# Kernel tuning notes

Hardware: AMD Instinct MI355X
Metric: run time of the kernel (lower is better)

## Reference

```python
import jax, jax.numpy as jnp
import numpy as np
import math

BLOCK = 256
NUM_HEADS = 32
HEAD_DIM = 128
HIDDEN = 2048
INNER = NUM_HEADS * HEAD_DIM
SEQ = 4096
EPS = 1e-5
LAYER_IDX = 0
NUM_LAYERS = 32


def _build_slopes(n):
    def get_slopes(n):
        def pow2(m):
            start = 2 ** (-2 ** (-(math.log2(m) - 3)))
            return [start * start ** i for i in range(m)]
        if math.log2(n).is_integer():
            return pow2(n)
        c = 2 ** math.floor(math.log2(n))
        return pow2(c) + get_slopes(2 * c)[0::2][: n - c]
    s = np.asarray(get_slopes(n), dtype=np.float32).reshape(n, 1, 1)
    # layer decay scaling as in __init__
    s = s * (1.0 - LAYER_IDX / (NUM_LAYERS - 1) + 1e-5)
    return s


def setup_inputs() -> dict:
    key = jax.random.key(0)
    k1, k2, k3, k4 = jax.random.split(key, 4)
    sd_h = 1.0 / math.sqrt(HIDDEN)
    sd_i = 1.0 / math.sqrt(INNER)
    return {
        "hidden_states": jax.random.normal(k1, (SEQ, HIDDEN), jnp.float32),
        "w_qkv": jax.random.normal(k2, (HIDDEN, 3 * INNER), jnp.float32) * sd_h,
        "w_gate": jax.random.normal(k3, (HIDDEN, INNER), jnp.float32) * sd_h,
        "w_out": jax.random.normal(k4, (INNER, HIDDEN), jnp.float32) * sd_i,
        "norm_weight": jnp.ones((INNER,), jnp.float32),
        "slope_rate": jnp.asarray(_build_slopes(NUM_HEADS)),
        "kv_cache": jnp.zeros((NUM_HEADS, HEAD_DIM, HEAD_DIM), jnp.float32),
    }


def _lightning_attention(q, k, v, slope, kv0):
    # q,k,v: [h, n, d]; slope: [h,1,1]; kv0: [h, d, d]
    h, n, d = q.shape
    nb = n // BLOCK
    qb = q.reshape(h, nb, BLOCK, d).transpose(1, 0, 2, 3)  # [nb,h,B,d]
    kb = k.reshape(h, nb, BLOCK, d).transpose(1, 0, 2, 3)
    vb = v.reshape(h, nb, BLOCK, d).transpose(1, 0, 2, 3)

    idx = jnp.arange(BLOCK, dtype=jnp.float32)
    diff = idx[:, None] - idx[None, :]                      # i - j
    s = slope.reshape(h, 1, 1)
    intra_decay = jnp.where(diff >= 0, jnp.exp(-s * diff), 0.0)   # [h,B,B]
    q_decay = jnp.exp(-s * (idx + 1.0).reshape(1, BLOCK, 1))      # [h,B,1]
    k_decay = jnp.exp(-s * (BLOCK - 1.0 - idx).reshape(1, BLOCK, 1))  # [h,B,1]
    block_decay = jnp.exp(-s * BLOCK)                             # [h,1,1]

    def step(kv, blk):
        qc, kc, vc = blk  # each [h,B,d]
        scores = jnp.einsum('hid,hjd->hij', qc, kc) * intra_decay
        o_intra = jnp.einsum('hij,hjd->hid', scores, vc)
        o_inter = q_decay * jnp.einsum('hid,hde->hie', qc, kv)
        kv_new = block_decay * kv + jnp.einsum('hjd,hje->hde', kc * k_decay, vc)
        return kv_new, o_intra + o_inter

    kv_final, outs = jax.lax.scan(step, kv0, (qb, kb, vb))
    out = outs.transpose(1, 0, 2, 3).reshape(h, n, d)
    return out, kv_final


def reference(hidden_states, w_qkv, w_gate, w_out, norm_weight, slope_rate, kv_cache):
    n = hidden_states.shape[0]
    # qkv projection + SiLU activation (done in fp32 in the original)
    qkv = jax.nn.silu(hidden_states @ w_qkv)                  # [n, 3*inner]
    qkv = qkv.reshape(n, NUM_HEADS, 3 * HEAD_DIM)
    q, k, v = jnp.split(qkv, 3, axis=-1)                      # [n,h,d] each
    q = q.transpose(1, 0, 2)                                  # [h,n,d]
    k = k.transpose(1, 0, 2)
    v = v.transpose(1, 0, 2)

    attn, kv_final = _lightning_attention(q, k, v, slope_rate, kv_cache)
    attn = attn.transpose(1, 0, 2).reshape(n, INNER)          # n (h d)

    # RMSNorm (fp32) then sigmoid gate then output projection
    var = jnp.mean(attn * attn, axis=-1, keepdims=True)
    normed = attn * jax.lax.rsqrt(var + EPS) * norm_weight
    gate = jax.nn.sigmoid(hidden_states @ w_gate)
    out = (gate * normed) @ w_out                             # [n, hidden]
    return out
```

## Files before the change

kernel.cpp:

```cpp
#include <hip/hip_runtime.h>
#include <stdint.h>

typedef __bf16 bf16x8 __attribute__((ext_vector_type(8)));
typedef float  f32x4  __attribute__((ext_vector_type(4)));
typedef unsigned short u16x8 __attribute__((ext_vector_type(8)));

__device__ __forceinline__ unsigned short f2bf(float f) {
    union { float f; uint32_t u; } x; x.f = f;
    uint32_t r = (x.u + 0x7FFFu + ((x.u >> 16) & 1u)) >> 16;
    return (unsigned short)r;
}
__device__ __forceinline__ float bf2f(unsigned short b) {
    union { uint32_t u; float f; } x; x.u = ((uint32_t)b) << 16;
    return x.f;
}

__device__ __forceinline__ void gl16(const void* g, void* l) {
    __builtin_amdgcn_global_load_lds(
        (const __attribute__((address_space(1))) void*)g,
        (__attribute__((address_space(3))) void*)(uint32_t)(uintptr_t)l,
        16, 0, 0);
}

#define MFMA16(a, b, c) __builtin_amdgcn_mfma_f32_16x16x32_bf16((a), (b), (c), 0, 0, 0)

__global__ __launch_bounds__(256) void f32_to_bf16_kernel(const float* __restrict__ in,
                                                          unsigned short* __restrict__ out,
                                                          int n8) {
    int i = blockIdx.x * 256 + threadIdx.x;
    if (i >= n8) return;
    float4 a = ((const float4*)in)[2 * i];
    float4 b = ((const float4*)in)[2 * i + 1];
    u16x8 o;
    o[0] = f2bf(a.x); o[1] = f2bf(a.y); o[2] = f2bf(a.z); o[3] = f2bf(a.w);
    o[4] = f2bf(b.x); o[5] = f2bf(b.y); o[6] = f2bf(b.z); o[7] = f2bf(b.w);
    ((u16x8*)out)[i] = o;
}

__global__ __launch_bounds__(256) void transpose_w_kernel(const float* __restrict__ in,
                                                          unsigned short* __restrict__ out,
                                                          int R, int C) {
    __shared__ float tile[64][65];
    int c0 = blockIdx.x * 64, r0 = blockIdx.y * 64;
    int tid = threadIdx.x;
    int tr = tid >> 4;
    int tc4 = (tid & 15) * 4;
#pragma unroll
    for (int it = 0; it < 4; ++it) {
        int r = it * 16 + tr;
        float4 v = *(const float4*)&in[(size_t)(r0 + r) * C + c0 + tc4];
        tile[r][tc4] = v.x; tile[r][tc4 + 1] = v.y;
        tile[r][tc4 + 2] = v.z; tile[r][tc4 + 3] = v.w;
    }
    __syncthreads();
#pragma unroll
    for (int it = 0; it < 4; ++it) {
        int c = it * 16 + tr;
        ushort4 o;
        o.x = f2bf(tile[tc4][c]);
        o.y = f2bf(tile[tc4 + 1][c]);
        o.z = f2bf(tile[tc4 + 2][c]);
        o.w = f2bf(tile[tc4 + 3][c]);
        *(ushort4*)&out[(size_t)(c0 + c) * R + r0 + tc4] = o;
    }
}

__global__ __launch_bounds__(512, 2) void gemm_qkvgate_kernel(const unsigned short* __restrict__ A,
                                                              const unsigned short* __restrict__ Bt,
                                                              unsigned short* __restrict__ qkvp,
                                                              unsigned short* __restrict__ gatep,
                                                              int K, int NBN, int NQ) {
    __shared__ unsigned short Abuf[2][2][8192];
    __shared__ unsigned short Bbuf[2][2][8192];

    int bid = blockIdx.x;
    int xcd = bid & 7, kw = bid >> 3;
    int bm = (xcd & 3) * 4 + (kw & 3);
    int bn = (xcd >> 2) * (NBN >> 1) + (kw >> 2);
    int tid = threadIdx.x, lane = tid & 63, w = tid >> 6;
    int wr = w >> 2, wc = w & 3;

    int r0 = tid >> 3;
    int cbs = (tid & 7) << 4;
    int el0 = (cbs ^ ((r0 & 7) << 4)) >> 1;
    int r1 = 64 + r0;
    int el1 = (cbs ^ ((r1 & 7) << 4)) >> 1;
    int lo0 = tid * 16, lo1 = 8192 + tid * 16;

    const unsigned short* Ag0 = A + (size_t)(bm * 256) * K;
    const unsigned short* Ag1 = A + (size_t)(bm * 256 + 128) * K;
    const unsigned short* Bg0 = Bt + (size_t)(bn * 256) * K;
    const unsigned short* Bg1 = Bt + (size_t)(bn * 256 + 128) * K;

#define STAGE(src, dstHalf, k0)                                            \
    do {                                                                   \
        gl16((src) + (size_t)r0 * K + (k0) + el0, (char*)(dstHalf) + lo0); \
        gl16((src) + (size_t)r1 * K + (k0) + el1, (char*)(dstHalf) + lo1); \
    } while (0)

    int aRow = wr * 64 + (lane & 15);
    int bRow = wc * 32 + (lane & 15);
    int swz = (lane & 7) << 4;
    int cbb = (lane >> 4) << 4;

#define RD_A(slot, R, m, kk) \
    af[R][m][kk] = *(const bf16x8*)((const char*)Abuf[slot][R] + ((aRow + (m) * 16) << 7) + (((kk) * 64 + cbb) ^ swz))
#define RD_B(slot, Cq, n, kk) \
    bfr[Cq][n][kk] = *(const bf16x8*)((const char*)Bbuf[slot][Cq] + ((bRow + (n) * 16) << 7) + (((kk) * 64 + cbb) ^ swz))

#define QUAD(q, Rh, Cc)                                                       \
    do {                                                                      \
        _Pragma("unroll")                                                     \
        for (int m = 0; m < 4; ++m)                                           \
            _Pragma("unroll")                                                 \
            for (int n = 0; n < 2; ++n) {                                     \
                acc[q][m][n] = MFMA16(af[Rh][m][0], bfr[Cc][n][0], acc[q][m][n]); \
                acc[q][m][n] = MFMA16(af[Rh][m][1], bfr[Cc][n][1], acc[q][m][n]); \
            }                                                                 \
    } while (0)

    bf16x8 af[2][4][2];
    bf16x8 bfr[2][2][2];
    f32x4 acc[4][4][2];
#pragma unroll
    for (int q = 0; q < 4; ++q)
#pragma unroll
        for (int m = 0; m < 4; ++m)
#pragma unroll
            for (int n = 0; n < 2; ++n)
#pragma unroll
                for (int r = 0; r < 4; ++r) acc[q][m][n][r] = 0.f;

    int NT = K >> 6;
    STAGE(Ag0, Abuf[0][0], 0);
    STAGE(Bg0, Bbuf[0][0], 0);
    STAGE(Ag1, Abuf[0][1], 0);
    STAGE(Bg1, Bbuf[0][1], 0);
    STAGE(Ag0, Abuf[1][0], 64);
    STAGE(Bg0, Bbuf[1][0], 64);
    STAGE(Ag1, Abuf[1][1], 64);
    STAGE(Bg1, Bbuf[1][1], 64);
    asm volatile("s_waitcnt vmcnt(8)" ::: "memory");
    __builtin_amdgcn_s_barrier();
#pragma unroll
    for (int m = 0; m < 4; ++m) { RD_A(0, 0, m, 0); RD_A(0, 0, m, 1); }
#pragma unroll
    for (int n = 0; n < 2; ++n) { RD_B(0, 0, n, 0); RD_B(0, 0, n, 1); }

    for (int t = 0; t < NT; ++t) {
        int cur = t & 1, nx = cur ^ 1;
        bool rd = (t + 1 < NT);
        bool st = (t + 2 < NT);
        int ks = (t + 2) << 6;

#pragma unroll
        for (int m = 0; m < 4; ++m) { RD_A(cur, 1, m, 0); RD_A(cur, 1, m, 1); }
        asm volatile("s_waitcnt lgkmcnt(8)" ::: "memory");
        __builtin_amdgcn_sched_barrier(0);
        __builtin_amdgcn_s_setprio(1);
        QUAD(0, 0, 0);
        __builtin_amdgcn_s_setprio(0);

#pragma unroll
        for (int n = 0; n < 2; ++n) { RD_B(cur, 1, n, 0); RD_B(cur, 1, n, 1); }
        asm volatile("s_waitcnt lgkmcnt(4)" ::: "memory");
        __builtin_amdgcn_sched_barrier(0);
        __builtin_amdgcn_s_setprio(1);
        QUAD(1, 1, 0);
        __builtin_amdgcn_s_setprio(0);

        asm volatile("s_waitcnt lgkmcnt(0)" ::: "memory");
        asm volatile("s_waitcnt vmcnt(0)" ::: "memory");
        __builtin_amdgcn_s_barrier();
        if (st) {
            STAGE(Ag0, Abuf[cur][0], ks);
            STAGE(Bg0, Bbuf[cur][0], ks);
        }
        if (rd) {
#pragma unroll
            for (int n = 0; n < 2; ++n) { RD_B(nx, 0, n, 0); RD_B(nx, 0, n, 1); }
        }
        __builtin_amdgcn_s_setprio(1);
        QUAD(2, 0, 1);
        __builtin_amdgcn_s_setprio(0);

        if (st) {
            STAGE(Ag1, Abuf[cur][1], ks);
            STAGE(Bg1, Bbuf[cur][1], ks);
        }
        if (rd) {
#pragma unroll
            for (int m = 0; m < 4; ++m) { RD_A(nx, 0, m, 0); RD_A(nx, 0, m, 1); }
        }
        __builtin_amdgcn_s_setprio(1);
        QUAD(3, 1, 1);
        __builtin_amdgcn_s_setprio(0);
    }

    bool isQ = (bn < NQ);
    unsigned short* outp = isQ ? qkvp : gatep;
    int Nout = isQ ? 12288 : 4096;
    int colb0 = (isQ ? bn : bn - NQ) * 256;
#pragma unroll
    for (int q = 0; q < 4; ++q) {
        const int R_ = q & 1, C_ = q >> 1;
#pragma unroll
        for (int m = 0; m < 4; ++m) {
            int row0 = bm * 256 + R_ * 128 + wr * 64 + m * 16 + ((lane >> 4) * 4);
#pragma unroll
            for (int n = 0; n < 2; ++n) {
                int col = colb0 + C_ * 128 + wc * 32 + n * 16 + (lane & 15);
#pragma unroll
                for (int rg = 0; rg < 4; ++rg) {
                    float v = acc[q][m][n][rg];
                    float sig = 1.f / (1.f + __expf(-v));
                    float r = isQ ? v * sig : sig;
                    outp[(size_t)(row0 + rg) * Nout + col] = f2bf(r);
                }
            }
        }
    }
#undef STAGE
#undef RD_A
#undef RD_B
#undef QUAD
}

template <int ACT, int OUTBF>
__global__ __launch_bounds__(256) void gemm_bt_kernel(const unsigned short* __restrict__ A,
                                                      const unsigned short* __restrict__ Bt,
                                                      void* __restrict__ Cp,
                                                      int M, int N, int K) {
    __shared__ unsigned short As[128 * 64];
    __shared__ unsigned short Bs[128 * 64];
    int bn = blockIdx.x, bm = blockIdx.y;
    int tid = threadIdx.x, lane = tid & 63, w = tid >> 6;
    int wr = w >> 1, wc = w & 1;

    f32x4 acc[4][4];
#pragma unroll
    for (int m = 0; m < 4; ++m)
#pragma unroll
        for (int n = 0; n < 4; ++n)
#pragma unroll
            for (int r = 0; r < 4; ++r) acc[m][n][r] = 0.f;

    const size_t Abase = (size_t)bm * 128 * K;
    const size_t Bbase = (size_t)bn * 128 * K;

    for (int k0 = 0; k0 < K; k0 += 64) {
        __syncthreads();
#pragma unroll
        for (int it = 0; it < 4; ++it) {
            int slot = it * 256 + tid;
            int o = slot * 16;
            int r = o >> 7;
            int cb = o & 127;
            int scb = cb ^ ((r & 7) << 4);
            gl16(A + Abase + (size_t)r * K + k0 + (scb >> 1), (char*)As + o);
            gl16(Bt + Bbase + (size_t)r * K + k0 + (scb >> 1), (char*)Bs + o);
        }
        __syncthreads();
#pragma unroll
        for (int kk = 0; kk < 2; ++kk) {
            int kb = kk * 64 + ((lane >> 4) * 16);
            bf16x8 af[4], bfr[4];
#pragma unroll
            for (int m = 0; m < 4; ++m) {
                int r = wr * 64 + m * 16 + (lane & 15);
                af[m] = *(const bf16x8*)((const char*)As + (r << 7) + (kb ^ ((r & 7) << 4)));
            }
#pragma unroll
            for (int n = 0; n < 4; ++n) {
                int r = wc * 64 + n * 16 + (lane & 15);
                bfr[n] = *(const bf16x8*)((const char*)Bs + (r << 7) + (kb ^ ((r & 7) << 4)));
            }
#pragma unroll
            for (int m = 0; m < 4; ++m)
#pragma unroll
                for (int n = 0; n < 4; ++n)
                    acc[m][n] = MFMA16(af[m], bfr[n], acc[m][n]);
        }
    }

#pragma unroll
    for (int m = 0; m < 4; ++m) {
        int rowb = bm * 128 + wr * 64 + m * 16 + ((lane >> 4) * 4);
#pragma unroll
        for (int n = 0; n < 4; ++n) {
            int col = bn * 128 + wc * 64 + n * 16 + (lane & 15);
#pragma unroll
            for (int r = 0; r < 4; ++r) {
                float v = acc[m][n][r];
                if (ACT == 1) v = v / (1.f + __expf(-v));
                else if (ACT == 2) v = 1.f / (1.f + __expf(-v));
                size_t idx = (size_t)(rowb + r) * N + col;
                if (OUTBF) ((unsigned short*)Cp)[idx] = f2bf(v);
                else       ((float*)Cp)[idx] = v;
            }
        }
    }
}

__global__ __launch_bounds__(256) void kv_transpose_kernel(const unsigned short* __restrict__ qkv,
                                                           const float* __restrict__ slopes,
                                                           unsigned short* __restrict__ kts,
                                                           unsigned short* __restrict__ vt) {
    __shared__ unsigned short tk[32][33];
    __shared__ unsigned short tv[32][33];
    int n0 = blockIdx.x * 32, d0 = blockIdx.y * 32, h = blockIdx.z;
    float s = slopes[h];
    int lx = threadIdx.x & 31, ly = threadIdx.x >> 5;
#pragma unroll
    for (int i = ly; i < 32; i += 8) {
        int n = n0 + i;
        size_t rowb = (size_t)n * 12288 + h * 384;
        float kv = bf2f(qkv[rowb + 128 + d0 + lx]) * __expf(-s * (float)(255 - (n & 255)));
        tk[i][lx] = f2bf(kv);
        tv[i][lx] = qkv[rowb + 256 + d0 + lx];
    }
    __syncthreads();
#pragma unroll
    for (int i = ly; i < 32; i += 8) {
        size_t ob = (size_t)(h * 128 + d0 + i) * 4096 + n0 + lx;
        kts[ob] = tk[lx][i];
        vt[ob] = tv[lx][i];
    }
}

__global__ __launch_bounds__(256) void kv_outer_kernel(const unsigned short* __restrict__ kts,
                                                       const unsigned short* __restrict__ vt,
                                                       float* __restrict__ U) {
    __shared__ unsigned short Kc[128 * 64];
    __shared__ unsigned short Vc[128 * 64];
    int blk = blockIdx.x;
    int h = blk & 31, t = blk >> 5;
    int tid = threadIdx.x, lane = tid & 63, w = tid >> 6;

    f32x4 acc[2][8];
#pragma unroll
    for (int m = 0; m < 2; ++m)
#pragma unroll
        for (int n = 0; n < 8; ++n)
#pragma unroll
            for (int r = 0; r < 4; ++r) acc[m][n][r] = 0.f;

    for (int ks = 0; ks < 4; ++ks) {
        __syncthreads();
#pragma unroll
        for (int it = 0; it < 4; ++it) {
            int slot = it * 256 + tid;
            int o = slot * 16;
            int r = o >> 7;
            int cb = o & 127;
            int scb = cb ^ ((r & 7) << 4);
            size_t j = (size_t)t * 256 + ks * 64 + (scb >> 1);
            gl16(kts + (size_t)(h * 128 + r) * 4096 + j, (char*)Kc + o);
            gl16(vt + (size_t)(h * 128 + r) * 4096 + j, (char*)Vc + o);
        }
        __syncthreads();
#pragma unroll
        for (int kk = 0; kk < 2; ++kk) {
            int kb = kk * 64 + ((lane >> 4) * 16);
            bf16x8 vf[2], kf[8];
#pragma unroll
            for (int m = 0; m < 2; ++m) {
                int e = w * 32 + m * 16 + (lane & 15);
                vf[m] = *(const bf16x8*)((const char*)Vc + (e << 7) + (kb ^ ((e & 7) << 4)));
            }
#pragma unroll
            for (int n = 0; n < 8; ++n) {
                int d = n * 16 + (lane & 15);
                kf[n] = *(const bf16x8*)((const char*)Kc + (d << 7) + (kb ^ ((d & 7) << 4)));
            }
#pragma unroll
            for (int m = 0; m < 2; ++m)
#pragma unroll
                for (int n = 0; n < 8; ++n)
                    acc[m][n] = MFMA16(vf[m], kf[n], acc[m][n]);
        }
    }
    size_t base = (size_t)(h * 16 + t) * 16384;
#pragma unroll
    for (int m = 0; m < 2; ++m)
#pragma unroll
        for (int n = 0; n < 8; ++n)
#pragma unroll
            for (int r = 0; r < 4; ++r) {
                int e = w * 32 + m * 16 + ((lane >> 4) * 4) + r;
                int d = n * 16 + (lane & 15);
                U[base + (size_t)e * 128 + d] = acc[m][n][r];
            }
}

__global__ __launch_bounds__(256) void kv_scan_kernel(const float* __restrict__ kv_cache,
                                                      const float* __restrict__ U,
                                                      const float* __restrict__ slopes,
                                                      unsigned short* __restrict__ Wb) {
    __shared__ float Tt[16][132];
    int h = blockIdx.x >> 3;
    int c = blockIdx.x & 7;
    int c0 = c * 2048, e0 = c * 16;
    int tid = threadIdx.x;
    float s = slopes[h];
    float bd = __expf(-s * 256.f);
    size_t hb = (size_t)h * 16384;
#pragma unroll
    for (int it = 0; it < 8; ++it) {
        int d = it * 16 + (tid >> 4);
        Tt[tid & 15][d] = kv_cache[hb + (size_t)d * 128 + e0 + (tid & 15)];
    }
    __syncthreads();
    float wst[8];
#pragma unroll
    for (int i = 0; i < 8; ++i) {
        int e_rel = i * 2 + (tid >> 7);
        wst[i] = Tt[e_rel][tid & 127];
    }
    for (int t = 0; t < 16; ++t) {
        size_t base = (size_t)(h * 16 + t) * 16384 + c0;
#pragma unroll
        for (int i = 0; i < 8; ++i) {
            int idx = i * 256 + tid;
            Wb[base + idx] = f2bf(wst[i]);
            wst[i] = bd * wst[i] + U[base + idx];
        }
    }
}

__global__ __launch_bounds__(256, 2) void attn_out_kernel(const unsigned short* __restrict__ qkv,
                                                          const unsigned short* __restrict__ vt,
                                                          const unsigned short* __restrict__ Wb,
                                                          const float* __restrict__ slopes,
                                                          unsigned short* __restrict__ attn) {
    __shared__ unsigned short lds[40960];
    unsigned short* Qs = lds;
    unsigned short* Ps = lds + 16384;
    unsigned short* KW = lds + 24576;
    unsigned short* Ks = KW;
    unsigned short* Vs = KW + 8192;

    int blk = blockIdx.x;
    int h = blk & 31, tq = blk >> 5;
    int t = tq >> 1, qh = tq & 1;
    float s = slopes[h];
    int tid = threadIdx.x, lane = tid & 63, w = tid >> 6;
    int rowbase = t * 256 + qh * 128;

#pragma unroll
    for (int it = 0; it < 8; ++it) {
        int o = (it * 256 + tid) * 16;
        int r = o >> 8, cb = o & 255, scb = cb ^ ((r & 7) << 4);
        gl16(qkv + (size_t)(rowbase + r) * 12288 + h * 384 + (scb >> 1), (char*)Qs + o);
    }
#pragma unroll
    for (int it = 0; it < 8; ++it) {
        int o = (it * 256 + tid) * 16;
        int e = o >> 8, cb = o & 255, scb = cb ^ ((e & 7) << 4);
        gl16(Wb + (size_t)((h * 16 + t) * 128 + e) * 128 + (scb >> 1), (char*)KW + o);
    }
    __syncthreads();

    f32x4 acc[2][8];
#pragma unroll
    for (int m = 0; m < 2; ++m)
#pragma unroll
        for (int n = 0; n < 8; ++n)
#pragma unroll
            for (int r = 0; r < 4; ++r) acc[m][n][r] = 0.f;

#pragma unroll
    for (int kk = 0; kk < 4; ++kk) {
        int kb = kk * 64 + ((lane >> 4) * 16);
        bf16x8 qf[2], wf[8];
#pragma unroll
        for (int m = 0; m < 2; ++m) {
            int r = w * 32 + m * 16 + (lane & 15);
            qf[m] = *(const bf16x8*)((const char*)Qs + (r << 8) + (kb ^ ((r & 7) << 4)));
        }
#pragma unroll
        for (int n = 0; n < 8; ++n) {
            int e = n * 16 + (lane & 15);
            wf[n] = *(const bf16x8*)((const char*)KW + (e << 8) + (kb ^ ((e & 7) << 4)));
        }
#pragma unroll
        for (int m = 0; m < 2; ++m)
#pragma unroll
            for (int n = 0; n < 8; ++n)
                acc[m][n] = MFMA16(qf[m], wf[n], acc[m][n]);
    }
#pragma unroll
    for (int m = 0; m < 2; ++m)
#pragma unroll
        for (int rg = 0; rg < 4; ++rg) {
            int i = qh * 128 + w * 32 + m * 16 + ((lane >> 4) * 4) + rg;
            float qd = __expf(-s * (float)(i + 1));
#pragma unroll
            for (int n = 0; n < 8; ++n) acc[m][n][rg] *= qd;
        }

    int jbmax = ((qh << 2) + w) >> 1;
    for (int jb = 0; jb < 4; ++jb) {
        __syncthreads();
#pragma unroll
        for (int it = 0; it < 4; ++it) {
            int o = (it * 256 + tid) * 16;
            int r = o >> 8, cb = o & 255, scb = cb ^ ((r & 7) << 4);
            gl16(qkv + (size_t)(t * 256 + jb * 64 + r) * 12288 + h * 384 + 128 + (scb >> 1),
                 (char*)Ks + o);
        }
#pragma unroll
        for (int it = 0; it < 4; ++it) {
            int o = (it * 256 + tid) * 16;
            int e = o >> 7, cb = o & 127, scb = cb ^ ((e & 7) << 4);
            gl16(vt + (size_t)(h * 128 + e) * 4096 + t * 256 + jb * 64 + (scb >> 1),
                 (char*)Vs + o);
        }
        __syncthreads();

        if (jb <= jbmax) {
            f32x4 sc[2][4];
#pragma unroll
            for (int m = 0; m < 2; ++m)
#pragma unroll
                for (int n = 0; n < 4; ++n)
#pragma unroll
                    for (int r = 0; r < 4; ++r) sc[m][n][r] = 0.f;
#pragma unroll
            for (int kk = 0; kk < 4; ++kk) {
                int kb = kk * 64 + ((lane >> 4) * 16);
                bf16x8 qf[2], kf[4];
#pragma unroll
                for (int m = 0; m < 2; ++m) {
                    int r = w * 32 + m * 16 + (lane & 15);
                    qf[m] = *(const bf16x8*)((const char*)Qs + (r << 8) + (kb ^ ((r & 7) << 4)));
                }
#pragma unroll
                for (int n = 0; n < 4; ++n) {
                    int r = n * 16 + (lane & 15);
                    kf[n] = *(const bf16x8*)((const char*)Ks + (r << 8) + (kb ^ ((r & 7) << 4)));
                }
#pragma unroll
                for (int m = 0; m < 2; ++m)
#pragma unroll
                    for (int n = 0; n < 4; ++n)
                        sc[m][n] = MFMA16(qf[m], kf[n], sc[m][n]);
            }
            unsigned short* Pw = Ps + w * 2048;
#pragma unroll
            for (int m = 0; m < 2; ++m)
#pragma unroll
                for (int n = 0; n < 4; ++n)
#pragma unroll
                    for (int rg = 0; rg < 4; ++rg) {
                        int il = m * 16 + ((lane >> 4) * 4) + rg;
                        int i = qh * 128 + w * 32 + il;
                        int jl = n * 16 + (lane & 15);
                        int j = jb * 64 + jl;
                        float v = 0.f;
                        if (i >= j) v = sc[m][n][rg] * __expf(-s * (float)(i - j));
                        int cb2 = (jl * 2) ^ ((il & 7) << 4);
                        *(unsigned short*)((char*)Pw + (il << 7) + cb2) = f2bf(v);
                    }
            asm volatile("s_waitcnt lgkmcnt(0)" ::: "memory");
#pragma unroll
            for (int kk = 0; kk < 2; ++kk) {
                int kb = kk * 64 + ((lane >> 4) * 16);
                bf16x8 pf[2], vf[8];
#pragma unroll
                for (int m = 0; m < 2; ++m) {
                    int il = m * 16 + (lane & 15);
                    pf[m] = *(const bf16x8*)((const char*)Pw + (il << 7) + (kb ^ ((il & 7) << 4)));
                }
#pragma unroll
                for (int n = 0; n < 8; ++n) {
                    int e = n * 16 + (lane & 15);
                    vf[n] = *(const bf16x8*)((const char*)Vs + (e << 7) + (kb ^ ((e & 7) << 4)));
                }
#pragma unroll
                for (int m = 0; m < 2; ++m)
#pragma unroll
                    for (int n = 0; n < 8; ++n)
                        acc[m][n] = MFMA16(pf[m], vf[n], acc[m][n]);
            }
        }
    }

#pragma unroll
    for (int m = 0; m < 2; ++m)
#pragma unroll
        for (int n = 0; n < 8; ++n)
#pragma unroll
            for (int rg = 0; rg < 4; ++rg) {
                int i = qh * 128 + w * 32 + m * 16 + ((lane >> 4) * 4) + rg;
                int col = h * 128 + n * 16 + (lane & 15);
                attn[(size_t)(t * 256 + i) * 4096 + col] = f2bf(acc[m][n][rg]);
            }
}

__global__ __launch_bounds__(256) void rms_gate_kernel(const unsigned short* __restrict__ attn,
                                                       const unsigned short* __restrict__ gate,
                                                       const float* __restrict__ nw,
                                                       unsigned short* __restrict__ gated) {
    int row = blockIdx.x, tid = threadIdx.x;
    int lane = tid & 63, w = tid >> 6;
    const unsigned short* ar = attn + (size_t)row * 4096 + tid * 16;
    u16x8 a0 = *(const u16x8*)ar;
    u16x8 a1 = *(const u16x8*)(ar + 8);
    float v[16];
    float ss = 0.f;
#pragma unroll
    for (int j = 0; j < 8; ++j) { v[j] = bf2f(a0[j]); v[8 + j] = bf2f(a1[j]); }
#pragma unroll
    for (int j = 0; j < 16; ++j) ss += v[j] * v[j];
#pragma unroll
    for (int o = 32; o > 0; o >>= 1) ss += __shfl_xor(ss, o);
    __shared__ float red[4];
    if (lane == 0) red[w] = ss;
    __syncthreads();
    float tot = red[0] + red[1] + red[2] + red[3];
    float rs = rsqrtf(tot * (1.f / 4096.f) + 1e-5f);
    const unsigned short* gr = gate + (size_t)row * 4096 + tid * 16;
    u16x8 g0 = *(const u16x8*)gr;
    u16x8 g1 = *(const u16x8*)(gr + 8);
    const float* nwp = nw + tid * 16;
    u16x8 o0, o1;
#pragma unroll
    for (int j = 0; j < 8; ++j) {
        o0[j] = f2bf(v[j] * rs * nwp[j] * bf2f(g0[j]));
        o1[j] = f2bf(v[8 + j] * rs * nwp[8 + j] * bf2f(g1[j]));
    }
    unsigned short* gp = gated + (size_t)row * 4096 + tid * 16;
    *(u16x8*)gp = o0;
    *(u16x8*)(gp + 8) = o1;
}

extern "C" void kernel_launch(void* const* d_in, const int* in_sizes, int n_in,
                              void* d_out, int out_size, void* d_ws, size_t ws_size,
                              hipStream_t stream) {
    const float* hs       = (const float*)d_in[0];
    const float* w_qkv    = (const float*)d_in[1];
    const float* w_gate   = (const float*)d_in[2];
    const float* w_out    = (const float*)d_in[3];
    const float* nw       = (const float*)d_in[4];
    const float* slopes   = (const float*)d_in[5];
    const float* kv_cache = (const float*)d_in[6];
    float* out = (float*)d_out;
    char* ws = (char*)d_ws;

    unsigned short* hsb  = (unsigned short*)(ws + 0);
    unsigned short* wqt  = (unsigned short*)(ws + 16777216);
    unsigned short* wgt  = (unsigned short*)(ws + 67108864);
    unsigned short* wot  = (unsigned short*)(ws + 83886080);
    unsigned short* qkv  = (unsigned short*)(ws + 100663296);
    unsigned short* gate = (unsigned short*)(ws + 201326592);
    unsigned short* kts  = (unsigned short*)(ws + 234881024);
    unsigned short* vt   = (unsigned short*)(ws + 268435456);
    float*          U    = (float*)(ws + 301989888);
    unsigned short* Wb   = (unsigned short*)(ws + 335544320);
    unsigned short* attn  = wqt;
    unsigned short* gated = qkv;

    f32_to_bf16_kernel<<<4096, 256, 0, stream>>>(hs, hsb, 1048576);
    {
        dim3 g(192, 32);
        transpose_w_kernel<<<g, 256, 0, stream>>>(w_qkv, wqt, 2048, 12288);
    }
    {
        dim3 g(64, 32);
        transpose_w_kernel<<<g, 256, 0, stream>>>(w_gate, wgt, 2048, 4096);
    }
    {
        dim3 g(32, 64);
        transpose_w_kernel<<<g, 256, 0, stream>>>(w_out, wot, 4096, 2048);
    }
    gemm_qkvgate_kernel<<<1024, 512, 0, stream>>>(hsb, wqt, qkv, gate, 2048, 64, 48);
    {
        dim3 g(128, 4, 32);
        kv_transpose_kernel<<<g, 256, 0, stream>>>(qkv, slopes, kts, vt);
    }
    kv_outer_kernel<<<512, 256, 0, stream>>>(kts, vt, U);
    kv_scan_kernel<<<256, 256, 0, stream>>>(kv_cache, U, slopes, Wb);
    attn_out_kernel<<<1024, 256, 0, stream>>>(qkv, vt, Wb, slopes, attn);
    rms_gate_kernel<<<4096, 256, 0, stream>>>(attn, gate, nw, gated);
    {
        dim3 g(16, 32);
        gemm_bt_kernel<0, 0><<<g, 256, 0, stream>>>(gated, wot, out, 4096, 2048, 4096);
    }
}
```

Baseline: 507.5 us.

## Pipeline output GEMM with double-buffered LDS and relax waitcnts in QKV GEMM

Replaces the simple single-buffered output projection GEMM with a double-buffered, quadrant-split kernel. It prefetches the next K tiles via global_load_lds while MFMAs run, raises occupancy to two blocks per CU, and remaps workgroup ids with an XCD-aware swizzle. In the fused QKV/gate GEMM, the full vmcnt(0) drain is replaced by partial waits plus an extra barrier at loop top, so loads for the next stage stay in flight longer. The added synchronisation and tighter vmcnt counting risk race conditions if the counts are off.

```diff
diff --git a/kernel.cpp b/kernel.cpp
--- a/kernel.cpp
+++ b/kernel.cpp
@@ -153,6 +153,12 @@
         bool st = (t + 2 < NT);
         int ks = (t + 2) << 6;
 
+        if (t) {
+            if (rd) asm volatile("s_waitcnt vmcnt(8)" ::: "memory");
+            else    asm volatile("s_waitcnt vmcnt(0)" ::: "memory");
+            __builtin_amdgcn_s_barrier();
+            __builtin_amdgcn_sched_barrier(0);
+        }
 #pragma unroll
         for (int m = 0; m < 4; ++m) { RD_A(cur, 1, m, 0); RD_A(cur, 1, m, 1); }
         asm volatile("s_waitcnt lgkmcnt(8)" ::: "memory");
@@ -170,8 +176,10 @@
         __builtin_amdgcn_s_setprio(0);
 
         asm volatile("s_waitcnt lgkmcnt(0)" ::: "memory");
-        asm volatile("s_waitcnt vmcnt(0)" ::: "memory");
+        if (rd) asm volatile("s_waitcnt vmcnt(4)" ::: "memory");
+        else    asm volatile("s_waitcnt vmcnt(0)" ::: "memory");
         __builtin_amdgcn_s_barrier();
+        __builtin_amdgcn_sched_barrier(0);
         if (st) {
             STAGE(Ag0, Abuf[cur][0], ks);
             STAGE(Bg0, Bbuf[cur][0], ks);
@@ -226,80 +234,163 @@
 #undef QUAD
 }
 
-template <int ACT, int OUTBF>
-__global__ __launch_bounds__(256) void gemm_bt_kernel(const unsigned short* __restrict__ A,
-                                                      const unsigned short* __restrict__ Bt,
-                                                      void* __restrict__ Cp,
-                                                      int M, int N, int K) {
-    __shared__ unsigned short As[128 * 64];
-    __shared__ unsigned short Bs[128 * 64];
-    int bn = blockIdx.x, bm = blockIdx.y;
+__global__ __launch_bounds__(256, 2) void gemm_out_kernel(const unsigned short* __restrict__ A,
+                                                          const unsigned short* __restrict__ Bt,
+                                                          float* __restrict__ Cout,
+                                                          int N, int K, int NBN) {
+    __shared__ unsigned short Abuf[2][2][4096];
+    __shared__ unsigned short Bbuf[2][2][4096];
+
+    int bid = blockIdx.x, nwg = gridDim.x;
+    int wg = (bid & 7) * (nwg >> 3) + (bid >> 3);
+    int bm = wg / NBN, bn = wg % NBN;
     int tid = threadIdx.x, lane = tid & 63, w = tid >> 6;
     int wr = w >> 1, wc = w & 1;
 
-    f32x4 acc[4][4];
-#pragma unroll
-    for (int m = 0; m < 4; ++m)
-#pragma unroll
-        for (int n = 0; n < 4; ++n)
-#pragma unroll
-            for (int r = 0; r < 4; ++r) acc[m][n][r] = 0.f;
-
-    const size_t Abase = (size_t)bm * 128 * K;
-    const size_t Bbase = (size_t)bn * 128 * K;
-
-    for (int k0 = 0; k0 < K; k0 += 64) {
-        __syncthreads();
-#pragma unroll
-        for (int it = 0; it < 4; ++it) {
-            int slot = it * 256 + tid;
-            int o = slot * 16;
-            int r = o >> 7;
-            int cb = o & 127;
-            int scb = cb ^ ((r & 7) << 4);
-            gl16(A + Abase + (size_t)r * K + k0 + (scb >> 1), (char*)As + o);
-            gl16(Bt + Bbase + (size_t)r * K + k0 + (scb >> 1), (char*)Bs + o);
-        }
-        __syncthreads();
-#pragma unroll
-        for (int kk = 0; kk < 2; ++kk) {
-            int kb = kk * 64 + ((lane >> 4) * 16);
-            bf16x8 af[4], bfr[4];
-#pragma unroll
-            for (int m = 0; m < 4; ++m) {
-                int r = wr * 64 + m * 16 + (lane & 15);
-                af[m] = *(const bf16x8*)((const char*)As + (r << 7) + (kb ^ ((r & 7) << 4)));
+    int r0 = tid >> 3;
+    int cbs = (tid & 7) << 4;
+    int el0 = (cbs ^ ((r0 & 7) << 4)) >> 1;
+    int r1 = 32 + r0;
+    int el1 = (cbs ^ ((r1 & 7) << 4)) >> 1;
+    int lo0 = tid * 16, lo1 = 4096 + tid * 16;
+
+    const unsigned short* Ag0 = A + (size_t)(bm * 128) * K;
+    const unsigned short* Ag1 = A + (size_t)(bm * 128 + 64) * K;
+    const unsigned short* Bg0 = Bt + (size_t)(bn * 128) * K;
+    const unsigned short* Bg1 = Bt + (size_t)(bn * 128 + 64) * K;
+
+#define STAGE(src, dstHalf, k0)                                            \
+    do {                                                                   \
+        gl16((src) + (size_t)r0 * K + (k0) + el0, (char*)(dstHalf) + lo0); \
+        gl16((src) + (size_t)r1 * K + (k0) + el1, (char*)(dstHalf) + lo1); \
+    } while (0)
+
+    int aRow = wr * 32 + (lane & 15);
+    int bRow = wc * 32 + (lane & 15);
+    int swz = (lane & 7) << 4;
+    int cbb = (lane >> 4) << 4;
+
+#define RD_A(slot, R, m, kk) \
+    af[R][m][kk] = *(const bf16x8*)((const char*)Abuf[slot][R] + ((aRow + (m) * 16) << 7) + (((kk) * 64 + cbb) ^ swz))
+#define RD_B(slot, Cq, n, kk) \
+    bfr[Cq][n][kk] = *(const bf16x8*)((const char*)Bbuf[slot][Cq] + ((bRow + (n) * 16) << 7) + (((kk) * 64 + cbb) ^ swz))
+
+#define QUAD(q, Rh, Cc)                                                       \
+    do {                                                                      \
+        _Pragma("unroll")                                                     \
+        for (int m = 0; m < 2; ++m)                                           \
+            _Pragma("unroll")                                                 \
+            for (int n = 0; n < 2; ++n) {                                     \
+                acc[q][m][n] = MFMA16(af[Rh][m][0], bfr[Cc][n][0], acc[q][m][n]); \
+                acc[q][m][n] = MFMA16(af[Rh][m][1], bfr[Cc][n][1], acc[q][m][n]); \
+            }                                                                 \
+    } while (0)
+
+    bf16x8 af[2][2][2];
+    bf16x8 bfr[2][2][2];
+    f32x4 acc[4][2][2];
+#pragma unroll
+    for (int q = 0; q < 4; ++q)
+#pragma unroll
+        for (int m = 0; m < 2; ++m)
+#pragma unroll
+            for (int n = 0; n < 2; ++n)
+#pragma unroll
+                for (int r = 0; r < 4; ++r) acc[q][m][n][r] = 0.f;
+
+    int NT = K >> 6;
+    STAGE(Ag0, Abuf[0][0], 0);
+    STAGE(Bg0, Bbuf[0][0], 0);
+    STAGE(Ag1, Abuf[0][1], 0);
+    STAGE(Bg1, Bbuf[0][1], 0);
+    STAGE(Ag0, Abuf[1][0], 64);
+    STAGE(Bg0, Bbuf[1][0], 64);
+    STAGE(Ag1, Abuf[1][1], 64);
+    STAGE(Bg1, Bbuf[1][1], 64);
+    asm volatile("s_waitcnt vmcnt(8)" ::: "memory");
+    __builtin_amdgcn_s_barrier();
+#pragma unroll
+    for (int m = 0; m < 2; ++m) { RD_A(0, 0, m, 0); RD_A(0, 0, m, 1); }
+#pragma unroll
+    for (int n = 0; n < 2; ++n) { RD_B(0, 0, n, 0); RD_B(0, 0, n, 1); }
+
+    for (int t = 0; t < NT; ++t) {
+        int cur = t & 1, nx = cur ^ 1;
+        bool rd = (t + 1 < NT);
+        bool st = (t + 2 < NT);
+        int ks = (t + 2) << 6;
+
+        if (t) {
+            if (rd) asm volatile("s_waitcnt vmcnt(8)" ::: "memory");
+            else    asm volatile("s_waitcnt vmcnt(0)" ::: "memory");
+            __builtin_amdgcn_s_barrier();
+            __builtin_amdgcn_sched_barrier(0);
+        }
+#pragma unroll
+        for (int m = 0; m < 2; ++m) { RD_A(cur, 1, m, 0); RD_A(cur, 1, m, 1); }
+        asm volatile("s_waitcnt lgkmcnt(4)" ::: "memory");
+        __builtin_amdgcn_sched_barrier(0);
+        __builtin_amdgcn_s_setprio(1);
+        QUAD(0, 0, 0);
+        __builtin_amdgcn_s_setprio(0);
+
+#pragma unroll
+        for (int n = 0; n < 2; ++n) { RD_B(cur, 1, n, 0); RD_B(cur, 1, n, 1); }
+        asm volatile("s_waitcnt lgkmcnt(4)" ::: "memory");
+        __builtin_amdgcn_sched_barrier(0);
+        __builtin_amdgcn_s_setprio(1);
+        QUAD(1, 1, 0);
+        __builtin_amdgcn_s_setprio(0);
+
+        asm volatile("s_waitcnt lgkmcnt(0)" ::: "memory");
+        if (rd) asm volatile("s_waitcnt vmcnt(4)" ::: "memory");
+        else    asm volatile("s_waitcnt vmcnt(0)" ::: "memory");
+        __builtin_amdgcn_s_barrier();
+        __builtin_amdgcn_sched_barrier(0);
+        if (st) {
+            STAGE(Ag0, Abuf[cur][0], ks);
+            STAGE(Bg0, Bbuf[cur][0], ks);
+        }
+        if (rd) {
+#pragma unroll
+            for (int n = 0; n < 2; ++n) { RD_B(nx, 0, n, 0); RD_B(nx, 0, n, 1); }
+        }
+        __builtin_amdgcn_s_setprio(1);
+        QUAD(2, 0, 1);
+        __builtin_amdgcn_s_setprio(0);
+
+        if (st) {
+            STAGE(Ag1, Abuf[cur][1], ks);
+            STAGE(Bg1, Bbuf[cur][1], ks);
+        }
+        if (rd) {
+#pragma unroll
+            for (int m = 0; m < 2; ++m) { RD_A(nx, 0, m, 0); RD_A(nx, 0, m, 1); }
+        }
+        __builtin_amdgcn_s_setprio(1);
+        QUAD(3, 1, 1);
+        __builtin_amdgcn_s_setprio(0);
+    }
+
+#pragma unroll
+    for (int q = 0; q < 4; ++q) {
+        const int R_ = q & 1, C_ = q >> 1;
+#pragma unroll
+        for (int m = 0; m < 2; ++m) {
+            int row0 = bm * 128 + R_ * 64 + wr * 32 + m * 16 + ((lane >> 4) * 4);
+#pragma unroll
+            for (int n = 0; n < 2; ++n) {
+                int col = bn * 128 + C_ * 64 + wc * 32 + n * 16 + (lane & 15);
+#pragma unroll
+                for (int rg = 0; rg < 4; ++rg)
+                    Cout[(size_t)(row0 + rg) * N + col] = acc[q][m][n][rg];
             }
-#pragma unroll
-            for (int n = 0; n < 4; ++n) {
-                int r = wc * 64 + n * 16 + (lane & 15);
-                bfr[n] = *(const bf16x8*)((const char*)Bs + (r << 7) + (kb ^ ((r & 7) << 4)));
-            }
-#pragma unroll
-            for (int m = 0; m < 4; ++m)
-#pragma unroll
-                for (int n = 0; n < 4; ++n)
-                    acc[m][n] = MFMA16(af[m], bfr[n], acc[m][n]);
-        }
-    }
-
-#pragma unroll
-    for (int m = 0; m < 4; ++m) {
-        int rowb = bm * 128 + wr * 64 + m * 16 + ((lane >> 4) * 4);
-#pragma unroll
-        for (int n = 0; n < 4; ++n) {
-            int col = bn * 128 + wc * 64 + n * 16 + (lane & 15);
-#pragma unroll
-            for (int r = 0; r < 4; ++r) {
-                float v = acc[m][n][r];
-                if (ACT == 1) v = v / (1.f + __expf(-v));
-                else if (ACT == 2) v = 1.f / (1.f + __expf(-v));
-                size_t idx = (size_t)(rowb + r) * N + col;
-                if (OUTBF) ((unsigned short*)Cp)[idx] = f2bf(v);
-                else       ((float*)Cp)[idx] = v;
-            }
-        }
-    }
+        }
+    }
+#undef STAGE
+#undef RD_A
+#undef RD_B
+#undef QUAD
 }
 
 __global__ __launch_bounds__(256) void kv_transpose_kernel(const unsigned short* __restrict__ qkv,
@@ -683,8 +774,5 @@
     kv_scan_kernel<<<256, 256, 0, stream>>>(kv_cache, U, slopes, Wb);
     attn_out_kernel<<<1024, 256, 0, stream>>>(qkv, vt, Wb, slopes, attn);
     rms_gate_kernel<<<4096, 256, 0, stream>>>(attn, gate, nw, gated);
-    {
-        dim3 g(16, 32);
-        gemm_bt_kernel<0, 0><<<g, 256, 0, stream>>>(gated, wot, out, 4096, 2048, 4096);
-    }
-}
+    gemm_out_kernel<<<512, 256, 0, stream>>>(gated, wot, out, 2048, 4096, 16);
+}
```

After: 490.7 us. 1.03x faster.
